# Kernel tuning notes

Hardware: AMD Instinct MI355X
Metric: run time of the kernel (lower is better)

The kernel has to match this reference:

```python
import jax, jax.numpy as jnp
import numpy as np

B, C, D, H, W = 1, 64, 24, 24, 24
N = D * H * W
K = D + H + W - 2  # cross neighbors per node (self deduped)
DS, GD = 64, 64    # d_sim, g_dim
GROUPS = C // 4
EPS = 1e-5
N_ITERS = 2        # pool_strides = [1, 1]


def _build_nbr_idx():
    i, j, k = np.meshgrid(np.arange(D), np.arange(H), np.arange(W), indexing='ij')
    i, j, k = i.reshape(-1), j.reshape(-1), k.reshape(-1)
    a0 = (j * W + k)[:, None] + np.arange(D)[None, :] * (H * W)      # (N, D) full depth line (incl self)
    full1 = (i * H * W + k)[:, None] + np.arange(H)[None, :] * W     # (N, H)
    a1 = full1[np.arange(H)[None, :] != j[:, None]].reshape(N, H - 1)
    full2 = (i * H * W + j * W)[:, None] + np.arange(W)[None, :]     # (N, W)
    a2 = full2[np.arange(W)[None, :] != k[:, None]].reshape(N, W - 1)
    return np.concatenate([a0, a1, a2], axis=1).astype(np.int32)     # (N, K)


def setup_inputs() -> dict:
    key = jax.random.key(0)
    ks = jax.random.split(key, 8)
    s = 0.05
    return {
        'x': jax.random.normal(ks[0], (B, C, D, H, W), jnp.float32),
        'nbr_idx': jnp.asarray(_build_nbr_idx()),
        'phi_w': jax.random.normal(ks[1], (DS, C), jnp.float32) * s,
        'phi_b': jnp.zeros((DS,), jnp.float32),
        'theta_w': jax.random.normal(ks[2], (DS, C), jnp.float32) * s,
        'theta_b': jnp.zeros((DS,), jnp.float32),
        'G_w': jax.random.normal(ks[3], (GD, C), jnp.float32) * s,
        'G_b': jnp.zeros((GD,), jnp.float32),
        'r_w': jax.random.normal(ks[4], (C, GD), jnp.float32) * s,
        'r_b': jnp.zeros((C,), jnp.float32),
        'gn_gamma': jnp.ones((N_ITERS, C), jnp.float32),
        'gn_beta': jnp.zeros((N_ITERS, C), jnp.float32),
        'bn_gamma': jnp.ones((C,), jnp.float32),
        'bn_beta': jnp.zeros((C,), jnp.float32),
        'bn_mean': jnp.zeros((C,), jnp.float32),
        'bn_var': jnp.ones((C,), jnp.float32),
    }


def _group_norm(v, gamma, beta):
    vg = v.reshape(B, GROUPS, C // GROUPS, D, H, W)
    m = vg.mean(axis=(2, 3, 4, 5), keepdims=True)
    var = ((vg - m) ** 2).mean(axis=(2, 3, 4, 5), keepdims=True)
    vn = ((vg - m) / jnp.sqrt(var + EPS)).reshape(B, C, D, H, W)
    return vn * gamma[None, :, None, None, None] + beta[None, :, None, None, None]


def reference(x, nbr_idx, phi_w, phi_b, theta_w, theta_b, G_w, G_b, r_w, r_b,
              gn_gamma, gn_beta, bn_gamma, bn_beta, bn_mean, bn_var):
    h = x
    for it in range(N_ITERS):
        hf = h.reshape(B, C, N).transpose(2, 0, 1)                    # (N, B, C) node features
        theta = jnp.einsum('nbc,dc->nbd', hf, theta_w) + theta_b     # (N, B, DS) queries
        phi_all = jnp.einsum('nbc,dc->nbd', hf, phi_w) + phi_b       # (N, B, DS) keys (pre-gather)
        g_all = jnp.einsum('nbc,gc->nbg', hf, G_w) + G_b             # (N, B, GD) values (pre-gather)
        phi_e = phi_all[nbr_idx]                                      # (N, K, B, DS) mailbox gather
        g_e = g_all[nbr_idx]                                          # (N, K, B, GD)
        f = jnp.einsum('nbd,nkbd->nbk', theta, phi_e)                # attention logits over K
        a = jax.nn.softmax(f, axis=-1)                                # non_local_merge 'softmax'
        y = jnp.einsum('nbk,nkbg->nbg', a, g_e)                      # weighted value sum
        cross = jnp.einsum('nbg,cg->nbc', y, r_w) + r_b              # (N, B, C) output proj
        cross = cross.transpose(1, 2, 0).reshape(B, C, D, H, W)
        h = h + _group_norm(cross, gn_gamma[it], gn_beta[it])
    # BatchNorm3d (eval, running stats) + ReLU
    bc = lambda v: v[None, :, None, None, None]
    out = (h - bc(bn_mean)) / jnp.sqrt(bc(bn_var) + EPS) * bc(bn_gamma) + bc(bn_beta)
    return jax.nn.relu(out)
```

## Files before the change

kernel.cpp:

```cpp
#include <hip/hip_runtime.h>
#include <math.h>

#define NN 13824
#define LW 24

__global__ __launch_bounds__(256) void apply_proj_kernel(
    const float* __restrict__ x,
    const float* __restrict__ cross, const float* __restrict__ gsum,
    const float* __restrict__ gn_g, const float* __restrict__ gn_b,
    float* __restrict__ h_out, int mode,
    const float* __restrict__ theta_w, const float* __restrict__ theta_b,
    const float* __restrict__ phi_w, const float* __restrict__ phi_b,
    const float* __restrict__ g_w, const float* __restrict__ g_b,
    float* __restrict__ theta, float* __restrict__ phi, float* __restrict__ gv)
{
    __shared__ float hs[64 * 64];
    __shared__ float ws[64 * 68];

    const int tid = threadIdx.x;
    const int tile = blockIdx.x / 3, ts = blockIdx.x % 3;
    const int n0 = tile * 64;

    const float* wsel = (ts == 0) ? theta_w : (ts == 1) ? phi_w : g_w;
    const float* bsel = (ts == 0) ? theta_b : (ts == 1) ? phi_b : g_b;
    float*       osel = (ts == 0) ? theta   : (ts == 1) ? phi   : gv;

    if (mode == 0) {
        for (int i = tid; i < 4096; i += 256) {
            int c = i >> 6, nl = i & 63;
            hs[c * 64 + nl] = x[(size_t)c * NN + n0 + nl];
        }
    } else {
        for (int i = tid; i < 4096; i += 256) {
            int nl = i >> 6, c = i & 63;
            ws[c * 68 + nl] = cross[(size_t)(n0 + nl) * 64 + c];
        }
        __syncthreads();
        const float inv_cnt = 1.f / 55296.f;
        for (int i = tid; i < 4096; i += 256) {
            int c = i >> 6, nl = i & 63;
            int gr = c >> 2;
            float mean = gsum[gr * 16] * inv_cnt;
            float var = gsum[512 + gr * 16] * inv_cnt - mean * mean;
            float v = (ws[c * 68 + nl] - mean) * rsqrtf(var + 1e-5f) * gn_g[c] + gn_b[c];
            size_t o = (size_t)c * NN + n0 + nl;
            float hv = x[o] + v;
            hs[c * 64 + nl] = hv;
            if (ts == 0) h_out[o] = hv;
        }
        __syncthreads();
    }

    for (int i = tid; i < 4096; i += 256) {
        int d = i >> 6, c = i & 63;
        ws[c * 68 + d] = wsel[d * 64 + c];
    }
    __syncthreads();

    const int d0  = (tid & 15) * 4;
    const int nl0 = (tid >> 4) * 4;
    float acc[4][4];
    #pragma unroll
    for (int q = 0; q < 4; q++)
        #pragma unroll
        for (int j = 0; j < 4; j++) acc[q][j] = 0.f;

    #pragma unroll 4
    for (int c = 0; c < 64; c++) {
        float4 hv = *(const float4*)&hs[c * 64 + nl0];
        float4 wv = *(const float4*)&ws[c * 68 + d0];
        #pragma unroll
        for (int j = 0; j < 4; j++) {
            float w = (&wv.x)[j];
            acc[0][j] += hv.x * w;
            acc[1][j] += hv.y * w;
            acc[2][j] += hv.z * w;
            acc[3][j] += hv.w * w;
        }
    }
    float4 bias = *(const float4*)&bsel[d0];
    #pragma unroll
    for (int q = 0; q < 4; q++) {
        float4 v;
        v.x = acc[q][0] + bias.x; v.y = acc[q][1] + bias.y;
        v.z = acc[q][2] + bias.z; v.w = acc[q][3] + bias.w;
        *(float4*)&osel[(size_t)(n0 + nl0 + q) * 64 + d0] = v;
    }
}

__global__ __launch_bounds__(128) void line_attn_kernel(
    const float* __restrict__ theta,
    const float* __restrict__ phi,
    const float* __restrict__ gv,
    float* __restrict__ y_part,
    float* __restrict__ l_part,
    float* __restrict__ gsum)
{
    __shared__ float th[2][LW * 68], ph[2][LW * 68], gs[2][LW * 68];
    __shared__ float P[2][LW * 28];

    const int tid = threadIdx.x;
    const int wv = tid >> 6, lane = tid & 63;
    const int gl = blockIdx.x * 2 + wv;
    const int axis = gl / 576, L = gl % 576;

    if (blockIdx.x == 0) {
        for (int i = tid; i < 1024; i += 128) gsum[i] = 0.f;
    }

    int base, stride;
    if (axis == 0)      { base = L * 24;                    stride = 1;   }
    else if (axis == 1) { base = (L / 24) * 576 + (L % 24); stride = 24;  }
    else                { base = L;                         stride = 576; }
    const bool excl = (axis != 2);

    #pragma unroll
    for (int q = 0; q < 6; q++) {
        int idx = q * 64 + lane;
        int row = idx >> 4, c4 = (idx & 15) * 4;
        size_t g = (size_t)(base + row * stride) * 64 + c4;
        int la = row * 68 + c4;
        *(float4*)&th[wv][la] = *(const float4*)&theta[g];
        *(float4*)&ph[wv][la] = *(const float4*)&phi[g];
        *(float4*)&gs[wv][la] = *(const float4*)&gv[g];
    }

    const int r0 = (lane >> 3) * 3, c0 = (lane & 7) * 3;
    float sa[3][3];
    #pragma unroll
    for (int a = 0; a < 3; a++)
        #pragma unroll
        for (int b = 0; b < 3; b++) sa[a][b] = 0.f;

    #pragma unroll 4
    for (int d4 = 0; d4 < 64; d4 += 4) {
        float4 t[3], p[3];
        #pragma unroll
        for (int a = 0; a < 3; a++) t[a] = *(const float4*)&th[wv][(r0 + a) * 68 + d4];
        #pragma unroll
        for (int b = 0; b < 3; b++) p[b] = *(const float4*)&ph[wv][(c0 + b) * 68 + d4];
        #pragma unroll
        for (int a = 0; a < 3; a++)
            #pragma unroll
            for (int b = 0; b < 3; b++)
                sa[a][b] += t[a].x * p[b].x + t[a].y * p[b].y +
                            t[a].z * p[b].z + t[a].w * p[b].w;
    }
    #pragma unroll
    for (int a = 0; a < 3; a++)
        #pragma unroll
        for (int b = 0; b < 3; b++) {
            float e = (excl && (r0 + a) == (c0 + b)) ? 0.f : __expf(sa[a][b]);
            P[wv][(r0 + a) * 28 + c0 + b] = e;
        }

    if (lane < 24) {
        float s = 0.f;
        #pragma unroll
        for (int c4 = 0; c4 < 24; c4 += 4) {
            float4 pv = *(const float4*)&P[wv][lane * 28 + c4];
            s += pv.x + pv.y + pv.z + pv.w;
        }
        l_part[(size_t)axis * NN + base + lane * stride] = s;
    }

    float acc[24];
    #pragma unroll
    for (int r = 0; r < 24; r++) acc[r] = 0.f;
    #pragma unroll
    for (int c4 = 0; c4 < 24; c4 += 4) {
        float g0 = gs[wv][(c4 + 0) * 68 + lane];
        float g1 = gs[wv][(c4 + 1) * 68 + lane];
        float g2 = gs[wv][(c4 + 2) * 68 + lane];
        float g3 = gs[wv][(c4 + 3) * 68 + lane];
        #pragma unroll
        for (int r = 0; r < 24; r++) {
            float4 pv = *(const float4*)&P[wv][r * 28 + c4];
            acc[r] += pv.x * g0 + pv.y * g1 + pv.z * g2 + pv.w * g3;
        }
    }
    float* yp = y_part + (size_t)axis * NN * 64;
    #pragma unroll
    for (int r = 0; r < 24; r++)
        yp[(size_t)(base + r * stride) * 64 + lane] = acc[r];
}

__global__ __launch_bounds__(256) void combine_kernel(
    const float* __restrict__ y_part, const float* __restrict__ l_part,
    const float* __restrict__ r_w, const float* __restrict__ r_b,
    float* __restrict__ cross, float* __restrict__ gsum)
{
    __shared__ float ys[16 * 68];
    __shared__ float red_s[4][64], red_ss[4][64];

    const int tid = threadIdx.x;
    const int d = tid & 63, w = tid >> 6;
    const int n0 = blockIdx.x * 16;
    const size_t S = (size_t)NN * 64;

    #pragma unroll
    for (int q = 0; q < 4; q++) {
        int nn = w * 4 + q;
        int n = n0 + nn;
        float lv = l_part[n] + l_part[NN + n] + l_part[2 * NN + n];
        size_t o = (size_t)n * 64 + d;
        float yv = y_part[o] + y_part[S + o] + y_part[2 * S + o];
        ys[nn * 68 + d] = yv / lv;
    }
    __syncthreads();

    const int c = d;
    float rb = r_b[c];
    float acc[4] = {rb, rb, rb, rb};
    for (int dd = 0; dd < 64; dd += 4) {
        float4 r4 = *(const float4*)&r_w[c * 64 + dd];
        #pragma unroll
        for (int q = 0; q < 4; q++) {
            float4 y4 = *(const float4*)&ys[(w * 4 + q) * 68 + dd];
            acc[q] += r4.x * y4.x + r4.y * y4.y + r4.z * y4.z + r4.w * y4.w;
        }
    }
    float s = 0.f, ss = 0.f;
    #pragma unroll
    for (int q = 0; q < 4; q++) {
        int n = n0 + w * 4 + q;
        cross[(size_t)n * 64 + c] = acc[q];
        s += acc[q];
        ss += acc[q] * acc[q];
    }
    red_s[w][c] = s;
    red_ss[w][c] = ss;
    __syncthreads();
    if (w == 0) {
        float ts  = red_s[0][c] + red_s[1][c] + red_s[2][c] + red_s[3][c];
        float tss = red_ss[0][c] + red_ss[1][c] + red_ss[2][c] + red_ss[3][c];
        ts  += __shfl_xor(ts, 1);  ts  += __shfl_xor(ts, 2);
        tss += __shfl_xor(tss, 1); tss += __shfl_xor(tss, 2);
        if ((c & 3) == 0) {
            atomicAdd(&gsum[(c >> 2) * 16], ts);
            atomicAdd(&gsum[512 + (c >> 2) * 16], tss);
        }
    }
}

__global__ __launch_bounds__(256) void final_kernel(
    const float* __restrict__ cross,
    const float* __restrict__ gsum,
    const float* __restrict__ gn_g, const float* __restrict__ gn_b,
    const float* __restrict__ h_in,
    const float* __restrict__ bn_g, const float* __restrict__ bn_b,
    const float* __restrict__ bn_m, const float* __restrict__ bn_v,
    float* __restrict__ out)
{
    __shared__ float t[64 * 65];
    const int tid = threadIdx.x;
    const int n0 = blockIdx.x * 64;
    for (int i = tid; i < 4096; i += 256) {
        int nl = i >> 6, c = i & 63;
        t[c * 65 + nl] = cross[(size_t)(n0 + nl) * 64 + c];
    }
    __syncthreads();
    const float inv_cnt = 1.f / 55296.f;
    for (int i = tid; i < 4096; i += 256) {
        int c = i >> 6, nl = i & 63;
        int gr = c >> 2;
        float mean = gsum[gr * 16] * inv_cnt;
        float var = gsum[512 + gr * 16] * inv_cnt - mean * mean;
        float v = (t[c * 65 + nl] - mean) * rsqrtf(var + 1e-5f) * gn_g[c] + gn_b[c];
        size_t o = (size_t)c * NN + n0 + nl;
        float h2 = h_in[o] + v;
        float bnv = (h2 - bn_m[c]) * rsqrtf(bn_v[c] + 1e-5f) * bn_g[c] + bn_b[c];
        out[o] = fmaxf(bnv, 0.f);
    }
}

extern "C" void kernel_launch(void* const* d_in, const int* in_sizes, int n_in,
                              void* d_out, int out_size, void* d_ws, size_t ws_size,
                              hipStream_t stream)
{
    const float* x        = (const float*)d_in[0];
    const float* phi_w    = (const float*)d_in[2];
    const float* phi_b    = (const float*)d_in[3];
    const float* theta_w  = (const float*)d_in[4];
    const float* theta_b  = (const float*)d_in[5];
    const float* G_w      = (const float*)d_in[6];
    const float* G_b      = (const float*)d_in[7];
    const float* r_w      = (const float*)d_in[8];
    const float* r_b      = (const float*)d_in[9];
    const float* gn_gamma = (const float*)d_in[10];
    const float* gn_beta  = (const float*)d_in[11];
    const float* bn_gamma = (const float*)d_in[12];
    const float* bn_beta  = (const float*)d_in[13];
    const float* bn_mean  = (const float*)d_in[14];
    const float* bn_var   = (const float*)d_in[15];

    float* ws = (float*)d_ws;
    const size_t S = (size_t)NN * 64;
    float* h1    = ws;
    float* theta = ws + S;
    float* phi   = ws + 2 * S;
    float* gv    = ws + 3 * S;
    float* ypart = ws + 4 * S;
    float* cross = ws + 7 * S;
    float* lpart = ws + 8 * S;
    float* gsum  = ws + 8 * S + 3 * NN;

    apply_proj_kernel<<<648, 256, 0, stream>>>(x, cross, gsum, gn_gamma, gn_beta,
                                               h1, 0,
                                               theta_w, theta_b, phi_w, phi_b,
                                               G_w, G_b, theta, phi, gv);
    line_attn_kernel<<<864, 128, 0, stream>>>(theta, phi, gv, ypart, lpart, gsum);
    combine_kernel<<<864, 256, 0, stream>>>(ypart, lpart, r_w, r_b, cross, gsum);
    apply_proj_kernel<<<648, 256, 0, stream>>>(x, cross, gsum, gn_gamma, gn_beta,
                                               h1, 1,
                                               theta_w, theta_b, phi_w, phi_b,
                                               G_w, G_b, theta, phi, gv);
    line_attn_kernel<<<864, 128, 0, stream>>>(theta, phi, gv, ypart, lpart, gsum);
    combine_kernel<<<864, 256, 0, stream>>>(ypart, lpart, r_w, r_b, cross, gsum);
    final_kernel<<<216, 256, 0, stream>>>(cross, gsum, gn_gamma + 64, gn_beta + 64,
                                          h1, bn_gamma, bn_beta, bn_mean, bn_var,
                                          (float*)d_out);
}
```

Baseline: 223.9 us.

## Fuse all stages into a persistent mega-kernel with software grid barriers

Replaces the seven separate launches with one persistent kernel of 512 blocks. The blocks synchronise through an atomic-counter grid barrier, and the residual h and cross tiles stay in LDS between phases. The theta/phi/g projections are merged into one interleaved 192-wide output, so each line load is a single gather, and the attention value step is retiled. The goal is to cut launch gaps and the global round-trips for h1/cross. The cost is that correctness depends on all 512 blocks being co-resident, and the LDS footprint is large.

```diff
diff --git a/kernel.cpp b/kernel.cpp
--- a/kernel.cpp
+++ b/kernel.cpp
@@ -2,143 +2,125 @@
 #include <math.h>
 
 #define NN 13824
-#define LW 24
-
-__global__ __launch_bounds__(256) void apply_proj_kernel(
-    const float* __restrict__ x,
-    const float* __restrict__ cross, const float* __restrict__ gsum,
-    const float* __restrict__ gn_g, const float* __restrict__ gn_b,
-    float* __restrict__ h_out, int mode,
-    const float* __restrict__ theta_w, const float* __restrict__ theta_b,
-    const float* __restrict__ phi_w, const float* __restrict__ phi_b,
-    const float* __restrict__ g_w, const float* __restrict__ g_b,
-    float* __restrict__ theta, float* __restrict__ phi, float* __restrict__ gv)
-{
-    __shared__ float hs[64 * 64];
-    __shared__ float ws[64 * 68];
-
-    const int tid = threadIdx.x;
-    const int tile = blockIdx.x / 3, ts = blockIdx.x % 3;
-    const int n0 = tile * 64;
-
-    const float* wsel = (ts == 0) ? theta_w : (ts == 1) ? phi_w : g_w;
-    const float* bsel = (ts == 0) ? theta_b : (ts == 1) ? phi_b : g_b;
-    float*       osel = (ts == 0) ? theta   : (ts == 1) ? phi   : gv;
-
-    if (mode == 0) {
-        for (int i = tid; i < 4096; i += 256) {
-            int c = i >> 6, nl = i & 63;
-            hs[c * 64 + nl] = x[(size_t)c * NN + n0 + nl];
-        }
-    } else {
-        for (int i = tid; i < 4096; i += 256) {
-            int nl = i >> 6, c = i & 63;
-            ws[c * 68 + nl] = cross[(size_t)(n0 + nl) * 64 + c];
-        }
-        __syncthreads();
-        const float inv_cnt = 1.f / 55296.f;
-        for (int i = tid; i < 4096; i += 256) {
-            int c = i >> 6, nl = i & 63;
-            int gr = c >> 2;
-            float mean = gsum[gr * 16] * inv_cnt;
-            float var = gsum[512 + gr * 16] * inv_cnt - mean * mean;
-            float v = (ws[c * 68 + nl] - mean) * rsqrtf(var + 1e-5f) * gn_g[c] + gn_b[c];
-            size_t o = (size_t)c * NN + n0 + nl;
-            float hv = x[o] + v;
-            hs[c * 64 + nl] = hv;
-            if (ts == 0) h_out[o] = hv;
-        }
-        __syncthreads();
-    }
-
-    for (int i = tid; i < 4096; i += 256) {
-        int d = i >> 6, c = i & 63;
-        ws[c * 68 + d] = wsel[d * 64 + c];
-    }
+#define SNODE 884736
+#define NTILE 432
+#define GRIDB 512
+#define INVC (1.0f / 55296.0f)
+
+__device__ __forceinline__ void gbar(unsigned* cnt, unsigned target) {
     __syncthreads();
-
-    const int d0  = (tid & 15) * 4;
-    const int nl0 = (tid >> 4) * 4;
-    float acc[4][4];
+    if (threadIdx.x == 0) {
+        __threadfence();
+        atomicAdd(cnt, 1u);
+        while (__hip_atomic_load(cnt, __ATOMIC_RELAXED, __HIP_MEMORY_SCOPE_AGENT) < target)
+            __builtin_amdgcn_s_sleep(2);
+        __threadfence();
+    }
+    __syncthreads();
+}
+
+
+__device__ __forceinline__ void stage_weights(
+    const float* __restrict__ tw, const float* __restrict__ pw,
+    const float* __restrict__ gw, float* wsm, int tid)
+{
+    #pragma unroll 4
+    for (int it = 0; it < 24; it++) {
+        int idx = it * 512 + tid * 4;
+        int d = idx >> 6, c4 = idx & 63;
+        const float* src = (d < 64) ? tw : (d < 128) ? pw : gw;
+        int dd = d & 63;
+        float4 w4 = *(const float4*)&src[dd * 64 + c4];
+        float a[4] = {w4.x, w4.y, w4.z, w4.w};
+        #pragma unroll
+        for (int j = 0; j < 4; j++) {
+            int jj = (j + tid) & 3;
+            wsm[(c4 + jj) * 196 + d] = a[jj];
+        }
+    }
+}
+
+__device__ __forceinline__ void proj_compute(
+    const float* hs, const float* wsm, const float* bias192,
+    float* __restrict__ tpg, int n0, int tid)
+{
+    const int dgrp = tid & 15, ngrp = tid >> 4;
+    const int d0 = dgrp * 12, nl0 = ngrp * 4;
+    float acc[4][12];
     #pragma unroll
     for (int q = 0; q < 4; q++)
         #pragma unroll
-        for (int j = 0; j < 4; j++) acc[q][j] = 0.f;
-
-    #pragma unroll 4
+        for (int j = 0; j < 12; j++) acc[q][j] = 0.f;
+
+    #pragma unroll 2
     for (int c = 0; c < 64; c++) {
-        float4 hv = *(const float4*)&hs[c * 64 + nl0];
-        float4 wv = *(const float4*)&ws[c * 68 + d0];
-        #pragma unroll
-        for (int j = 0; j < 4; j++) {
-            float w = (&wv.x)[j];
-            acc[0][j] += hv.x * w;
-            acc[1][j] += hv.y * w;
-            acc[2][j] += hv.z * w;
-            acc[3][j] += hv.w * w;
-        }
-    }
-    float4 bias = *(const float4*)&bsel[d0];
+        float4 hv = *(const float4*)&hs[c * 36 + nl0];
+        float w[12];
+        *(float4*)&w[0] = *(const float4*)&wsm[c * 196 + d0];
+        *(float4*)&w[4] = *(const float4*)&wsm[c * 196 + d0 + 4];
+        *(float4*)&w[8] = *(const float4*)&wsm[c * 196 + d0 + 8];
+        #pragma unroll
+        for (int j = 0; j < 12; j++) {
+            acc[0][j] += hv.x * w[j];
+            acc[1][j] += hv.y * w[j];
+            acc[2][j] += hv.z * w[j];
+            acc[3][j] += hv.w * w[j];
+        }
+    }
+    float b[12];
+    *(float4*)&b[0] = *(const float4*)&bias192[d0];
+    *(float4*)&b[4] = *(const float4*)&bias192[d0 + 4];
+    *(float4*)&b[8] = *(const float4*)&bias192[d0 + 8];
     #pragma unroll
     for (int q = 0; q < 4; q++) {
-        float4 v;
-        v.x = acc[q][0] + bias.x; v.y = acc[q][1] + bias.y;
-        v.z = acc[q][2] + bias.z; v.w = acc[q][3] + bias.w;
-        *(float4*)&osel[(size_t)(n0 + nl0 + q) * 64 + d0] = v;
-    }
-}
-
-__global__ __launch_bounds__(128) void line_attn_kernel(
-    const float* __restrict__ theta,
-    const float* __restrict__ phi,
-    const float* __restrict__ gv,
-    float* __restrict__ y_part,
-    float* __restrict__ l_part,
-    float* __restrict__ gsum)
-{
-    __shared__ float th[2][LW * 68], ph[2][LW * 68], gs[2][LW * 68];
-    __shared__ float P[2][LW * 28];
-
-    const int tid = threadIdx.x;
-    const int wv = tid >> 6, lane = tid & 63;
-    const int gl = blockIdx.x * 2 + wv;
-    const int axis = gl / 576, L = gl % 576;
-
-    if (blockIdx.x == 0) {
-        for (int i = tid; i < 1024; i += 128) gsum[i] = 0.f;
-    }
-
+        float* o = tpg + (size_t)(n0 + nl0 + q) * 192 + d0;
+        #pragma unroll
+        for (int k = 0; k < 3; k++) {
+            float4 v;
+            v.x = acc[q][4*k]   + b[4*k];
+            v.y = acc[q][4*k+1] + b[4*k+1];
+            v.z = acc[q][4*k+2] + b[4*k+2];
+            v.w = acc[q][4*k+3] + b[4*k+3];
+            *(float4*)&o[4*k] = v;
+        }
+    }
+}
+
+__device__ __forceinline__ void attn_line(
+    const float* __restrict__ tpg, float* __restrict__ ypart,
+    float* __restrict__ lpart, float* buf, float* P, int line, int lane)
+{
+    const int axis = line / 576, L = line % 576;
     int base, stride;
     if (axis == 0)      { base = L * 24;                    stride = 1;   }
     else if (axis == 1) { base = (L / 24) * 576 + (L % 24); stride = 24;  }
     else                { base = L;                         stride = 576; }
     const bool excl = (axis != 2);
 
-    #pragma unroll
-    for (int q = 0; q < 6; q++) {
+    __threadfence_block();
+    #pragma unroll 3
+    for (int q = 0; q < 18; q++) {
         int idx = q * 64 + lane;
-        int row = idx >> 4, c4 = (idx & 15) * 4;
-        size_t g = (size_t)(base + row * stride) * 64 + c4;
-        int la = row * 68 + c4;
-        *(float4*)&th[wv][la] = *(const float4*)&theta[g];
-        *(float4*)&ph[wv][la] = *(const float4*)&phi[g];
-        *(float4*)&gs[wv][la] = *(const float4*)&gv[g];
-    }
-
-    const int r0 = (lane >> 3) * 3, c0 = (lane & 7) * 3;
+        int row = idx / 48, ch = (idx % 48) * 4;
+        *(float4*)&buf[row * 196 + ch] =
+            *(const float4*)&tpg[(size_t)(base + row * stride) * 192 + ch];
+    }
+    __threadfence_block();
+
+    const int li = lane >> 3, lj = lane & 7;
+    const int r0 = li * 3, c0 = lj * 3;
     float sa[3][3];
     #pragma unroll
     for (int a = 0; a < 3; a++)
         #pragma unroll
         for (int b = 0; b < 3; b++) sa[a][b] = 0.f;
-
     #pragma unroll 4
     for (int d4 = 0; d4 < 64; d4 += 4) {
         float4 t[3], p[3];
         #pragma unroll
-        for (int a = 0; a < 3; a++) t[a] = *(const float4*)&th[wv][(r0 + a) * 68 + d4];
-        #pragma unroll
-        for (int b = 0; b < 3; b++) p[b] = *(const float4*)&ph[wv][(c0 + b) * 68 + d4];
+        for (int a = 0; a < 3; a++) t[a] = *(const float4*)&buf[(r0 + a) * 196 + d4];
+        #pragma unroll
+        for (int b = 0; b < 3; b++) p[b] = *(const float4*)&buf[(c0 + b) * 196 + 64 + d4];
         #pragma unroll
         for (int a = 0; a < 3; a++)
             #pragma unroll
@@ -146,131 +128,223 @@
                 sa[a][b] += t[a].x * p[b].x + t[a].y * p[b].y +
                             t[a].z * p[b].z + t[a].w * p[b].w;
     }
+    float rs[3] = {0.f, 0.f, 0.f};
     #pragma unroll
     for (int a = 0; a < 3; a++)
         #pragma unroll
         for (int b = 0; b < 3; b++) {
             float e = (excl && (r0 + a) == (c0 + b)) ? 0.f : __expf(sa[a][b]);
-            P[wv][(r0 + a) * 28 + c0 + b] = e;
-        }
-
-    if (lane < 24) {
-        float s = 0.f;
-        #pragma unroll
-        for (int c4 = 0; c4 < 24; c4 += 4) {
-            float4 pv = *(const float4*)&P[wv][lane * 28 + c4];
-            s += pv.x + pv.y + pv.z + pv.w;
-        }
-        l_part[(size_t)axis * NN + base + lane * stride] = s;
-    }
-
-    float acc[24];
-    #pragma unroll
-    for (int r = 0; r < 24; r++) acc[r] = 0.f;
-    #pragma unroll
-    for (int c4 = 0; c4 < 24; c4 += 4) {
-        float g0 = gs[wv][(c4 + 0) * 68 + lane];
-        float g1 = gs[wv][(c4 + 1) * 68 + lane];
-        float g2 = gs[wv][(c4 + 2) * 68 + lane];
-        float g3 = gs[wv][(c4 + 3) * 68 + lane];
-        #pragma unroll
-        for (int r = 0; r < 24; r++) {
-            float4 pv = *(const float4*)&P[wv][r * 28 + c4];
-            acc[r] += pv.x * g0 + pv.y * g1 + pv.z * g2 + pv.w * g3;
-        }
-    }
-    float* yp = y_part + (size_t)axis * NN * 64;
-    #pragma unroll
-    for (int r = 0; r < 24; r++)
-        yp[(size_t)(base + r * stride) * 64 + lane] = acc[r];
-}
-
-__global__ __launch_bounds__(256) void combine_kernel(
-    const float* __restrict__ y_part, const float* __restrict__ l_part,
+            rs[a] += e;
+            P[(r0 + a) * 28 + c0 + b] = e;
+        }
+    #pragma unroll
+    for (int off = 1; off <= 4; off <<= 1)
+        #pragma unroll
+        for (int a = 0; a < 3; a++) rs[a] += __shfl_xor(rs[a], off);
+    if (lj == 0) {
+        #pragma unroll
+        for (int a = 0; a < 3; a++)
+            lpart[(size_t)axis * NN + base + (r0 + a) * stride] = rs[a];
+    }
+    __threadfence_block();
+
+    const int rg = lane >> 4, dg = lane & 15;
+    float acc[6][4];
+    #pragma unroll
+    for (int i = 0; i < 6; i++)
+        #pragma unroll
+        for (int k = 0; k < 4; k++) acc[i][k] = 0.f;
+    #pragma unroll 4
+    for (int c = 0; c < 24; c++) {
+        float4 gv = *(const float4*)&buf[c * 196 + 128 + dg * 4];
+        #pragma unroll
+        for (int i = 0; i < 6; i++) {
+            float p = P[(rg * 6 + i) * 28 + c];
+            acc[i][0] += p * gv.x; acc[i][1] += p * gv.y;
+            acc[i][2] += p * gv.z; acc[i][3] += p * gv.w;
+        }
+    }
+    float* yp = ypart + (size_t)axis * SNODE;
+    #pragma unroll
+    for (int i = 0; i < 6; i++) {
+        float4 v = {acc[i][0], acc[i][1], acc[i][2], acc[i][3]};
+        *(float4*)&yp[(size_t)(base + (rg * 6 + i) * stride) * 64 + dg * 4] = v;
+    }
+}
+
+__device__ __forceinline__ void combine_phase(
+    const float* __restrict__ ypart, const float* __restrict__ lpart,
     const float* __restrict__ r_w, const float* __restrict__ r_b,
-    float* __restrict__ cross, float* __restrict__ gsum)
-{
-    __shared__ float ys[16 * 68];
-    __shared__ float red_s[4][64], red_ss[4][64];
+    float* ysL, float* crossL, float* red, float* gsum, int n0, int tid)
+{
+    const int wv = tid >> 6, lane = tid & 63;
+    #pragma unroll
+    for (int i = 0; i < 4; i++) {
+        int idx = i * 512 + tid * 4;
+        int nl = idx >> 6, d4 = idx & 63;
+        int n = n0 + nl;
+        float lv = lpart[n] + lpart[NN + n] + lpart[2 * NN + n];
+        float4 a = *(const float4*)&ypart[(size_t)n * 64 + d4];
+        float4 b = *(const float4*)&ypart[SNODE + (size_t)n * 64 + d4];
+        float4 c = *(const float4*)&ypart[2 * SNODE + (size_t)n * 64 + d4];
+        float inv = 1.f / lv;
+        float4 v = {(a.x + b.x + c.x) * inv, (a.y + b.y + c.y) * inv,
+                    (a.z + b.z + c.z) * inv, (a.w + b.w + c.w) * inv};
+        *(float4*)&ysL[nl * 68 + d4] = v;
+    }
+    __syncthreads();
+    const int cg = tid & 15, g = tid >> 4;
+    float acc[4][4];
+    #pragma unroll
+    for (int m = 0; m < 4; m++)
+        #pragma unroll
+        for (int j = 0; j < 4; j++) acc[m][j] = 0.f;
+    #pragma unroll 2
+    for (int dd = 0; dd < 64; dd += 4) {
+        float4 rw[4], ys[4];
+        #pragma unroll
+        for (int j = 0; j < 4; j++) rw[j] = *(const float4*)&r_w[(cg * 4 + j) * 64 + dd];
+        #pragma unroll
+        for (int m = 0; m < 4; m++) ys[m] = *(const float4*)&ysL[(g + 8 * m) * 68 + dd];
+        #pragma unroll
+        for (int m = 0; m < 4; m++)
+            #pragma unroll
+            for (int j = 0; j < 4; j++)
+                acc[m][j] += ys[m].x * rw[j].x + ys[m].y * rw[j].y +
+                             ys[m].z * rw[j].z + ys[m].w * rw[j].w;
+    }
+    float s = 0.f, ss = 0.f;
+    #pragma unroll
+    for (int m = 0; m < 4; m++)
+        #pragma unroll
+        for (int j = 0; j < 4; j++) {
+            float v = acc[m][j] + r_b[cg * 4 + j];
+            crossL[(cg * 4 + j) * 36 + g + 8 * m] = v;
+            s += v; ss += v * v;
+        }
+    s  += __shfl_xor(s, 16);  s  += __shfl_xor(s, 32);
+    ss += __shfl_xor(ss, 16); ss += __shfl_xor(ss, 32);
+    if (lane < 16) { red[wv * 32 + lane] = s; red[wv * 32 + 16 + lane] = ss; }
+    __syncthreads();
+    if (tid < 16) {
+        atomicAdd(&gsum[tid * 16],       red[tid] + red[32 + tid]);
+        atomicAdd(&gsum[512 + tid * 16], red[16 + tid] + red[48 + tid]);
+    }
+}
+
+__global__ void __launch_bounds__(128) zero_kernel(float* g, unsigned* cnt) {
+    int t = blockIdx.x * 128 + threadIdx.x;
+    g[t] = 0.f;
+    if (t == 0) *cnt = 0u;
+}
+
+__global__ void __launch_bounds__(128) mega_kernel(
+    const float* __restrict__ x,
+    const float* __restrict__ theta_w, const float* __restrict__ theta_b,
+    const float* __restrict__ phi_w,   const float* __restrict__ phi_b,
+    const float* __restrict__ g_w,     const float* __restrict__ g_b,
+    const float* __restrict__ r_w,     const float* __restrict__ r_b,
+    const float* __restrict__ gn_g,    const float* __restrict__ gn_b,
+    const float* __restrict__ bn_g,    const float* __restrict__ bn_b,
+    const float* __restrict__ bn_m,    const float* __restrict__ bn_v,
+    float* __restrict__ tpg, float* __restrict__ ypart, float* __restrict__ lpart,
+    float* __restrict__ gsumA, float* __restrict__ gsumB,
+    unsigned* __restrict__ cnt, float* __restrict__ out)
+{
+    __shared__ float lds[15040];
+    float* hs      = lds;
+    float* wsm     = lds + 2304;
+    float* crossL  = lds + 2304;
+    float* ysL     = lds + 4608;
+    float* red     = lds + 6784;
+    float* bias192 = lds + 14848;
 
     const int tid = threadIdx.x;
-    const int d = tid & 63, w = tid >> 6;
-    const int n0 = blockIdx.x * 16;
-    const size_t S = (size_t)NN * 64;
-
-    #pragma unroll
-    for (int q = 0; q < 4; q++) {
-        int nn = w * 4 + q;
-        int n = n0 + nn;
-        float lv = l_part[n] + l_part[NN + n] + l_part[2 * NN + n];
-        size_t o = (size_t)n * 64 + d;
-        float yv = y_part[o] + y_part[S + o] + y_part[2 * S + o];
-        ys[nn * 68 + d] = yv / lv;
-    }
-    __syncthreads();
-
-    const int c = d;
-    float rb = r_b[c];
-    float acc[4] = {rb, rb, rb, rb};
-    for (int dd = 0; dd < 64; dd += 4) {
-        float4 r4 = *(const float4*)&r_w[c * 64 + dd];
-        #pragma unroll
-        for (int q = 0; q < 4; q++) {
-            float4 y4 = *(const float4*)&ys[(w * 4 + q) * 68 + dd];
-            acc[q] += r4.x * y4.x + r4.y * y4.y + r4.z * y4.z + r4.w * y4.w;
-        }
-    }
-    float s = 0.f, ss = 0.f;
-    #pragma unroll
-    for (int q = 0; q < 4; q++) {
-        int n = n0 + w * 4 + q;
-        cross[(size_t)n * 64 + c] = acc[q];
-        s += acc[q];
-        ss += acc[q] * acc[q];
-    }
-    red_s[w][c] = s;
-    red_ss[w][c] = ss;
-    __syncthreads();
-    if (w == 0) {
-        float ts  = red_s[0][c] + red_s[1][c] + red_s[2][c] + red_s[3][c];
-        float tss = red_ss[0][c] + red_ss[1][c] + red_ss[2][c] + red_ss[3][c];
-        ts  += __shfl_xor(ts, 1);  ts  += __shfl_xor(ts, 2);
-        tss += __shfl_xor(tss, 1); tss += __shfl_xor(tss, 2);
-        if ((c & 3) == 0) {
-            atomicAdd(&gsum[(c >> 2) * 16], ts);
-            atomicAdd(&gsum[512 + (c >> 2) * 16], tss);
-        }
-    }
-}
-
-__global__ __launch_bounds__(256) void final_kernel(
-    const float* __restrict__ cross,
-    const float* __restrict__ gsum,
-    const float* __restrict__ gn_g, const float* __restrict__ gn_b,
-    const float* __restrict__ h_in,
-    const float* __restrict__ bn_g, const float* __restrict__ bn_b,
-    const float* __restrict__ bn_m, const float* __restrict__ bn_v,
-    float* __restrict__ out)
-{
-    __shared__ float t[64 * 65];
-    const int tid = threadIdx.x;
-    const int n0 = blockIdx.x * 64;
-    for (int i = tid; i < 4096; i += 256) {
-        int nl = i >> 6, c = i & 63;
-        t[c * 65 + nl] = cross[(size_t)(n0 + nl) * 64 + c];
-    }
-    __syncthreads();
-    const float inv_cnt = 1.f / 55296.f;
-    for (int i = tid; i < 4096; i += 256) {
-        int c = i >> 6, nl = i & 63;
-        int gr = c >> 2;
-        float mean = gsum[gr * 16] * inv_cnt;
-        float var = gsum[512 + gr * 16] * inv_cnt - mean * mean;
-        float v = (t[c * 65 + nl] - mean) * rsqrtf(var + 1e-5f) * gn_g[c] + gn_b[c];
-        size_t o = (size_t)c * NN + n0 + nl;
-        float h2 = h_in[o] + v;
-        float bnv = (h2 - bn_m[c]) * rsqrtf(bn_v[c] + 1e-5f) * bn_g[c] + bn_b[c];
-        out[o] = fmaxf(bnv, 0.f);
+    const int blk = blockIdx.x;
+    const int wv = tid >> 6, lane = tid & 63;
+    const int n0 = blk * 32;
+    float* abuf = lds + 2304 + wv * 5376;
+    float* aP   = abuf + 4704;
+
+    if (blk < NTILE) {
+        int c0 = tid >> 3, q4 = (tid & 7) * 4;
+        #pragma unroll
+        for (int cc = 0; cc < 64; cc += 16)
+            *(float4*)&hs[(c0 + cc) * 36 + q4] =
+                *(const float4*)&x[(size_t)(c0 + cc) * NN + n0 + q4];
+        stage_weights(theta_w, phi_w, g_w, wsm, tid);
+        if (tid < 64) {
+            bias192[tid] = theta_b[tid];
+            bias192[64 + tid] = phi_b[tid];
+            bias192[128 + tid] = g_b[tid];
+        }
+        __syncthreads();
+        proj_compute(hs, wsm, bias192, tpg, n0, tid);
+    }
+    gbar(cnt, 1 * GRIDB);
+
+    for (int pass = 0; pass < 2; pass++) {
+        int line = pass * 1024 + blk * 2 + wv;
+        if (line < 1728) attn_line(tpg, ypart, lpart, abuf, aP, line, lane);
+    }
+    gbar(cnt, 2 * GRIDB);
+
+    if (blk < NTILE) combine_phase(ypart, lpart, r_w, r_b, ysL, crossL, red, gsumA, n0, tid);
+    gbar(cnt, 3 * GRIDB);
+
+    if (blk < NTILE) {
+        #pragma unroll
+        for (int i = 0; i < 4; i++) {
+            int idx = i * 512 + tid * 4;
+            int c = idx >> 5, nlo = idx & 31;
+            int gr = c >> 2;
+            float mean = gsumA[gr * 16] * INVC;
+            float var  = gsumA[512 + gr * 16] * INVC - mean * mean;
+            float sc = rsqrtf(var + 1e-5f) * gn_g[c];
+            float sh = gn_b[c] - mean * sc;
+            float4 cr = *(const float4*)&crossL[c * 36 + nlo];
+            float4 h  = *(const float4*)&hs[c * 36 + nlo];
+            h.x += cr.x * sc + sh; h.y += cr.y * sc + sh;
+            h.z += cr.z * sc + sh; h.w += cr.w * sc + sh;
+            *(float4*)&hs[c * 36 + nlo] = h;
+        }
+        __syncthreads();
+        stage_weights(theta_w, phi_w, g_w, wsm, tid);
+        __syncthreads();
+        proj_compute(hs, wsm, bias192, tpg, n0, tid);
+    }
+    gbar(cnt, 4 * GRIDB);
+
+    for (int pass = 0; pass < 2; pass++) {
+        int line = pass * 1024 + blk * 2 + wv;
+        if (line < 1728) attn_line(tpg, ypart, lpart, abuf, aP, line, lane);
+    }
+    gbar(cnt, 5 * GRIDB);
+
+    if (blk < NTILE) combine_phase(ypart, lpart, r_w, r_b, ysL, crossL, red, gsumB, n0, tid);
+    gbar(cnt, 6 * GRIDB);
+
+    if (blk < NTILE) {
+        #pragma unroll
+        for (int i = 0; i < 4; i++) {
+            int idx = i * 512 + tid * 4;
+            int c = idx >> 5, nlo = idx & 31;
+            int gr = c >> 2;
+            float mean = gsumB[gr * 16] * INVC;
+            float var  = gsumB[512 + gr * 16] * INVC - mean * mean;
+            float sc = rsqrtf(var + 1e-5f) * gn_g[64 + c];
+            float sh = gn_b[64 + c] - mean * sc;
+            float bsc = rsqrtf(bn_v[c] + 1e-5f) * bn_g[c];
+            float bsh = bn_b[c] - bn_m[c] * bsc;
+            float4 cr = *(const float4*)&crossL[c * 36 + nlo];
+            float4 h  = *(const float4*)&hs[c * 36 + nlo];
+            float4 o;
+            o.x = fmaxf((h.x + cr.x * sc + sh) * bsc + bsh, 0.f);
+            o.y = fmaxf((h.y + cr.y * sc + sh) * bsc + bsh, 0.f);
+            o.z = fmaxf((h.z + cr.z * sc + sh) * bsc + bsh, 0.f);
+            o.w = fmaxf((h.w + cr.w * sc + sh) * bsc + bsh, 0.f);
+            *(float4*)&out[(size_t)c * NN + n0 + nlo] = o;
+        }
     }
 }
 
@@ -295,29 +369,16 @@
     const float* bn_var   = (const float*)d_in[15];
 
     float* ws = (float*)d_ws;
-    const size_t S = (size_t)NN * 64;
-    float* h1    = ws;
-    float* theta = ws + S;
-    float* phi   = ws + 2 * S;
-    float* gv    = ws + 3 * S;
-    float* ypart = ws + 4 * S;
-    float* cross = ws + 7 * S;
-    float* lpart = ws + 8 * S;
-    float* gsum  = ws + 8 * S + 3 * NN;
-
-    apply_proj_kernel<<<648, 256, 0, stream>>>(x, cross, gsum, gn_gamma, gn_beta,
-                                               h1, 0,
-                                               theta_w, theta_b, phi_w, phi_b,
-                                               G_w, G_b, theta, phi, gv);
-    line_attn_kernel<<<864, 128, 0, stream>>>(theta, phi, gv, ypart, lpart, gsum);
-    combine_kernel<<<864, 256, 0, stream>>>(ypart, lpart, r_w, r_b, cross, gsum);
-    apply_proj_kernel<<<648, 256, 0, stream>>>(x, cross, gsum, gn_gamma, gn_beta,
-                                               h1, 1,
-                                               theta_w, theta_b, phi_w, phi_b,
-                                               G_w, G_b, theta, phi, gv);
-    line_attn_kernel<<<864, 128, 0, stream>>>(theta, phi, gv, ypart, lpart, gsum);
-    combine_kernel<<<864, 256, 0, stream>>>(ypart, lpart, r_w, r_b, cross, gsum);
-    final_kernel<<<216, 256, 0, stream>>>(cross, gsum, gn_gamma + 64, gn_beta + 64,
-                                          h1, bn_gamma, bn_beta, bn_mean, bn_var,
-                                          (float*)d_out);
-}
+    float* tpg   = ws;
+    float* ypart = ws + 2654208;
+    float* lpart = ws + 5308416;
+    float* gsumA = ws + 5349888;
+    float* gsumB = ws + 5350912;
+    unsigned* cnt = (unsigned*)(ws + 5351936);
+
+    zero_kernel<<<16, 128, 0, stream>>>(gsumA, cnt);
+    mega_kernel<<<GRIDB, 128, 0, stream>>>(
+        x, theta_w, theta_b, phi_w, phi_b, G_w, G_b, r_w, r_b,
+        gn_gamma, gn_beta, bn_gamma, bn_beta, bn_mean, bn_var,
+        tpg, ypart, lpart, gsumA, gsumB, cnt, (float*)d_out);
+}
```

New measurement: 503.7 us. 125% more time.
